# Kernel optimization log

Measured on AMD Instinct MI355X. Metric: run time of the kernel, lower is better.

Reference implementation:

```python
import jax, jax.numpy as jnp
import numpy as np

N = 207      # node_size (METR-LA)
E = 1722     # edge_size from edge CSV
RES = 12     # resolution
T = 288 // RES  # time-of-day slots


def setup_inputs() -> dict:
    key = jax.random.key(0)
    ks = jax.random.split(key, 12)
    B, L = 64, 2048
    return {
        "inputs": jax.random.normal(ks[0], (B, 2, N, L), jnp.float32),
        "ind": jax.random.randint(ks[1], (B,), 0, 288),
        "edge_from": jax.random.randint(ks[2], (E,), 0, N),
        "edge_to": jax.random.randint(ks[3], (E,), 0, N),
        "weight_react": jax.random.normal(ks[4], (T, E), jnp.float32) / 10.0,
        "weight_diff": jax.random.normal(ks[5], (T, E), jnp.float32) / 1000.0,
        "weight_react_a": jax.random.normal(ks[6], (T, E), jnp.float32) / 10.0,
        "weight_diff_a": jax.random.normal(ks[7], (T, E), jnp.float32) / 1000.0,
        "bias_reaction": jax.random.normal(ks[8], (T, N), jnp.float32) / 10.0,
        "bias_diffusion": jax.random.normal(ks[9], (T, N), jnp.float32) / 10.0,
        "bias_reaction_a": jax.random.normal(ks[10], (T, N), jnp.float32) / 10.0,
        "bias_diffusion_a": jax.random.normal(ks[11], (T, N), jnp.float32) / 10.0,
    }


def _scatter(w, src, dst):
    # dense NxN from edge list; duplicate edges accumulate (torch sparse coalesce semantics)
    return jnp.zeros((N, N), w.dtype).at[src, dst].add(w)


def _diag_colsum(A):
    # torch.sum(A, 1) on [1,N,N] sums over the first node axis -> column sums
    return jax.vmap(jnp.diag)(A.sum(axis=1))


def reference(inputs, ind, edge_from, edge_to,
              weight_react, weight_diff, weight_react_a, weight_diff_a,
              bias_reaction, bias_diffusion, bias_reaction_a, bias_diffusion_a):
    x = inputs[:, 0, :, :]              # [B, N, L]
    ii = ind // RES                      # [B] time-slot indices

    scat = jax.vmap(_scatter, in_axes=(0, None, None))
    Ar = scat(weight_react[ii], edge_from, edge_to)      # [B,N,N] index = (i, j)
    Ad = scat(weight_diff[ii], edge_to, edge_from)       # index_a = (j, i)
    Ara = scat(weight_react_a[ii], edge_from, edge_to)
    Ada = scat(weight_diff_a[ii], edge_to, edge_from)

    RW = _diag_colsum(Ar) - Ar           # Laplacian: D - A
    DW = _diag_colsum(Ad) - Ad
    RWa = _diag_colsum(Ara) + Ara        # D + A
    # faithful replication: batch element 0 uses diag of colsums of the already-built
    # reaction Laplacian (I1 - A) instead of reaction_weight_a (original-code quirk)
    RWa = RWa.at[0].set(jnp.diag(RW[0].sum(axis=0)) + Ara[0])
    DWa = _diag_colsum(Ada) + Ada

    conv = lambda A: jnp.einsum('nvl,nwv->nwl', x, A)   # out[n,w,l] = sum_v A[n,w,v] x[n,v,l]
    reaction = conv(RW) + bias_reaction[ii][:, :, None]
    reaction_a = conv(RWa) + bias_reaction_a[ii][:, :, None]
    diffusion = conv(DW) + bias_diffusion[ii][:, :, None]
    diffusion_a = conv(DWa) + bias_diffusion_a[ii][:, :, None]

    return jnp.tanh(reaction) + jnp.tanh(reaction_a) + diffusion + diffusion_a + x
```

## Files before the change

kernel.cpp:

```cpp
#include <hip/hip_runtime.h>
#include <cstdint>
#include <cstddef>

#define NN 207
#define NE 1722
#define NT 24
#define LL 2048
#define LCC 128
#define KP  208
#define MTILES 13
#define KTILES 7
#define CH_U16 3584
#define T_U16 (MTILES * 3 * CH_U16)


typedef float    f32x4 __attribute__((ext_vector_type(4)));
typedef _Float16 half8 __attribute__((ext_vector_type(8)));

__device__ __forceinline__ unsigned short f2h(float f) {
    return __builtin_bit_cast(unsigned short, (_Float16)f);
}
__device__ __forceinline__ float tanhfast(float z) {
    return 1.0f - __fdividef(2.0f, __expf(2.0f * z) + 1.0f);
}

__global__ void k_build(const int* __restrict__ efrom, const int* __restrict__ eto,
                        const float* __restrict__ wr, const float* __restrict__ wd,
                        const float* __restrict__ wra, const float* __restrict__ wda,
                        const float* __restrict__ br, const float* __restrict__ bd,
                        const float* __restrict__ bra, const float* __restrict__ bda,
                        unsigned short* __restrict__ Wpack,
                        float4* __restrict__ cb4, float4* __restrict__ bb4) {
    const int t   = blockIdx.x / MTILES;
    const int mt  = blockIdx.x % MTILES;
    const int tid = threadIdx.x;
    __shared__ float rowbuf[3][16][KP];
    __shared__ float cs[4][16];

    float* rb = &rowbuf[0][0][0];
    for (int i = tid; i < 3 * 16 * KP; i += 256) rb[i] = 0.0f;
    if (tid < 64) ((float*)cs)[tid] = 0.0f;
    __syncthreads();

    const int mt16 = mt * 16;
    const float* wrt  = wr  + (size_t)t * NE;
    const float* wdt  = wd  + (size_t)t * NE;
    const float* wrat = wra + (size_t)t * NE;
    const float* wdat = wda + (size_t)t * NE;
    for (int e = tid; e < NE; e += 256) {
        int ef = efrom[e], et = eto[e];
        unsigned rf = (unsigned)(ef - mt16), rt = (unsigned)(et - mt16);
        bool in_f = rf < 16u, in_t = rt < 16u;
        if (in_f || in_t) {
            float w1 = wrt[e], w2 = wdt[e], w3 = wrat[e], w4 = wdat[e];
            if (in_t) {
                atomicAdd(&rowbuf[2][rt][ef], w4 - w2);
                atomicAdd(&cs[0][rt], w1);
                atomicAdd(&cs[1][rt], w3);
            }
            if (in_f) {
                atomicAdd(&rowbuf[0][rf][et], -w1);
                atomicAdd(&rowbuf[1][rf][et],  w3);
                atomicAdd(&cs[2][rf], w2);
                atomicAdd(&cs[3][rf], w4);
            }
        }
    }
    __syncthreads();

    if (tid < 16) {
        int w = mt16 + tid;
        if (w < NN) {
            cb4[t * NN + w] = make_float4(cs[0][tid], cs[1][tid], cs[2][tid] + cs[3][tid], 0.0f);
            bb4[t * NN + w] = make_float4(br[t * NN + w], bra[t * NN + w],
                                          bd[t * NN + w] + bda[t * NN + w], 0.0f);
        }
    }

    for (int fr = tid; fr < 3 * KTILES * 64; fr += 256) {
        int mat = fr / (KTILES * 64);
        int rem = fr - mat * (KTILES * 64);
        int ks = rem >> 6, lq = rem & 63;
        int r = lq & 15, g = lq >> 4;
        const float* src = &rowbuf[mat][r][0];
        int k0 = ks * 32 + 4 * g;
        unsigned short h[8];
        #pragma unroll
        for (int e2 = 0; e2 < 4; ++e2) {
            h[e2] = f2h(src[k0 + e2]);
            int kb = k0 + 16 + e2;
            h[4 + e2] = (kb < KP) ? f2h(src[kb]) : (unsigned short)0;
        }
        uint4 pv;
        pv.x = (unsigned)h[0] | ((unsigned)h[1] << 16);
        pv.y = (unsigned)h[2] | ((unsigned)h[3] << 16);
        pv.z = (unsigned)h[4] | ((unsigned)h[5] << 16);
        pv.w = (unsigned)h[6] | ((unsigned)h[7] << 16);
        size_t o = ((size_t)(t * MTILES + mt) * 3 + mat) * CH_U16 + (size_t)ks * 512 + (size_t)lq * 8;
        *(uint4*)(Wpack + o) = pv;
    }
}

__global__ __launch_bounds__(512, 4) void k_mfma(
    const float* __restrict__ inputs, const int* __restrict__ ind,
    const unsigned short* __restrict__ Wpack,
    const float4* __restrict__ cb4, const float4* __restrict__ bb4,
    float* __restrict__ out) {
    __shared__ unsigned short xs[KP * LCC];
    const int b = blockIdx.y, chunk = blockIdx.x, tid = threadIdx.x;
    const int t = ind[b] / 12;

    if (tid < 64) ((unsigned*)(xs + 207 * LCC))[tid] = 0u;

    const float* xb = inputs + (size_t)b * (2 * NN * LL) + (size_t)chunk * LCC;
    for (int i = tid; i < 207 * 32; i += 512) {
        int k  = i >> 5;
        int c4 = (i & 31) << 2;
        float4 v = *(const float4*)(xb + (size_t)k * LL + c4);
        int gk = (k >> 2) & 3;
        ushort4 h;
        h.x = f2h(v.x); h.y = f2h(v.y); h.z = f2h(v.z); h.w = f2h(v.w);
        *(ushort4*)&xs[k * LCC + (c4 ^ (gk << 4))] = h;
    }
    __syncthreads();

    const int l  = tid & 63, wv = tid >> 6;
    const int r  = l & 15,  g  = l >> 4;
    const int col  = wv * 16 + r;
    const int colx = col ^ (g << 4);
    const _Float16* xh = (const _Float16*)xs;

    half8 bf[KTILES];
    #pragma unroll
    for (int ks = 0; ks < KTILES - 1; ++ks) {
        half8 v;
        int k0 = ks * 32 + 4 * g;
        #pragma unroll
        for (int e = 0; e < 4; ++e) {
            v[e]     = xh[(k0 + e) * LCC + colx];
            v[4 + e] = xh[(k0 + 16 + e) * LCC + colx];
        }
        bf[ks] = v;
    }
    {
        half8 v = {0, 0, 0, 0, 0, 0, 0, 0};
        int k0 = 192 + 4 * g;
        #pragma unroll
        for (int e = 0; e < 4; ++e) v[e] = xh[(k0 + e) * LCC + colx];
        bf[KTILES - 1] = v;
    }

    const unsigned short* Ap = Wpack + (size_t)t * T_U16 + (size_t)l * 8;
    const float4* cbp = cb4 + (size_t)t * NN;
    const float4* bbp = bb4 + (size_t)t * NN;
    float* ob = out + (size_t)b * ((size_t)NN * LL) + (size_t)chunk * LCC + col;

    for (int mt = 0; mt < MTILES; ++mt) {
        f32x4 aR = {0.f, 0.f, 0.f, 0.f};
        f32x4 aA = {0.f, 0.f, 0.f, 0.f};
        f32x4 aD = {0.f, 0.f, 0.f, 0.f};
        #pragma unroll
        for (int ks = 0; ks < KTILES; ++ks) {
            half8 a = __builtin_bit_cast(half8, *(const uint4*)(Ap + ks * 512));
            aR = __builtin_amdgcn_mfma_f32_16x16x32_f16(a, bf[ks], aR, 0, 0, 0);
        }
        #pragma unroll
        for (int ks = 0; ks < KTILES; ++ks) {
            half8 a = __builtin_bit_cast(half8, *(const uint4*)(Ap + CH_U16 + ks * 512));
            aA = __builtin_amdgcn_mfma_f32_16x16x32_f16(a, bf[ks], aA, 0, 0, 0);
        }
        #pragma unroll
        for (int ks = 0; ks < KTILES; ++ks) {
            half8 a = __builtin_bit_cast(half8, *(const uint4*)(Ap + 2 * CH_U16 + ks * 512));
            aD = __builtin_amdgcn_mfma_f32_16x16x32_f16(a, bf[ks], aD, 0, 0, 0);
        }
        Ap += 3 * CH_U16;

        const int rowb = mt * 16 + 4 * g;
        #pragma unroll
        for (int q = 0; q < 4; ++q) {
            int row = rowb + q;
            if (row < NN) {
                float xq = (float)xh[row * LCC + colx];
                float4 cb = cbp[row], bb = bbp[row];
                float rr = aR[q] + cb.x * xq + bb.x;
                float ra = aA[q] + bb.y;
                if (b != 0) ra += cb.y * xq;
                float dd = aD[q] + cb.z * xq + bb.z;
                ob[(size_t)row * LL] = tanhfast(rr) + tanhfast(ra) + dd + xq;
            }
        }
    }
}

extern "C" void kernel_launch(void* const* d_in, const int* in_sizes, int n_in,
                              void* d_out, int out_size, void* d_ws, size_t ws_size,
                              hipStream_t stream) {
    const float* inputs = (const float*)d_in[0];
    const int*   ind    = (const int*)d_in[1];
    const int*   efrom  = (const int*)d_in[2];
    const int*   eto    = (const int*)d_in[3];
    const float* wr     = (const float*)d_in[4];
    const float* wd     = (const float*)d_in[5];
    const float* wra    = (const float*)d_in[6];
    const float* wda    = (const float*)d_in[7];
    const float* br     = (const float*)d_in[8];
    const float* bd     = (const float*)d_in[9];
    const float* bra    = (const float*)d_in[10];
    const float* bda    = (const float*)d_in[11];
    float* out = (float*)d_out;

    char* ws = (char*)d_ws;
    float4*         cb4   = (float4*)(ws + 0);
    float4*         bb4   = (float4*)(ws + 79488);
    unsigned short* Wpack = (unsigned short*)(ws + 158976);

    const int B = in_sizes[1];

    k_build<<<dim3(NT * MTILES), dim3(256), 0, stream>>>(
        efrom, eto, wr, wd, wra, wda, br, bd, bra, bda, Wpack, cb4, bb4);
    k_mfma<<<dim3(LL / LCC, B), dim3(512), 0, stream>>>(
        inputs, ind, Wpack, cb4, bb4, out);
}
```

Measured before the change: 421.6 us.

## Stage x through small per-k-slice LDS buffer and reuse fragments for epilogue

Replaces the full 208x128 fp16 LDS tile with a 32-row staging buffer that is filled and consumed once per k-slice, cutting LDS use from about 53KB to 8KB so more blocks can be resident per CU. The epilogue now takes the residual x value from the already-loaded B fragments instead of rereading LDS, and the m-tile loop is fully unrolled so those fragment indices are compile-time constants. The cost is two barriers per k-slice and serialized global loads with less overlap, plus higher register pressure and code size from the unroll.

```diff
diff --git a/kernel.cpp b/kernel.cpp
--- a/kernel.cpp
+++ b/kernel.cpp
@@ -106,48 +106,40 @@
     const unsigned short* __restrict__ Wpack,
     const float4* __restrict__ cb4, const float4* __restrict__ bb4,
     float* __restrict__ out) {
-    __shared__ unsigned short xs[KP * LCC];
+    __shared__ unsigned short sl[32 * LCC];
     const int b = blockIdx.y, chunk = blockIdx.x, tid = threadIdx.x;
     const int t = ind[b] / 12;
-
-    if (tid < 64) ((unsigned*)(xs + 207 * LCC))[tid] = 0u;
-
-    const float* xb = inputs + (size_t)b * (2 * NN * LL) + (size_t)chunk * LCC;
-    for (int i = tid; i < 207 * 32; i += 512) {
-        int k  = i >> 5;
-        int c4 = (i & 31) << 2;
-        float4 v = *(const float4*)(xb + (size_t)k * LL + c4);
-        int gk = (k >> 2) & 3;
-        ushort4 h;
-        h.x = f2h(v.x); h.y = f2h(v.y); h.z = f2h(v.z); h.w = f2h(v.w);
-        *(ushort4*)&xs[k * LCC + (c4 ^ (gk << 4))] = h;
-    }
-    __syncthreads();
 
     const int l  = tid & 63, wv = tid >> 6;
     const int r  = l & 15,  g  = l >> 4;
     const int col  = wv * 16 + r;
     const int colx = col ^ (g << 4);
-    const _Float16* xh = (const _Float16*)xs;
+    const _Float16* sh = (const _Float16*)sl;
+    const float* xb = inputs + (size_t)b * (2 * NN * LL) + (size_t)chunk * LCC;
 
     half8 bf[KTILES];
-    #pragma unroll
-    for (int ks = 0; ks < KTILES - 1; ++ks) {
+    for (int ks = 0; ks < KTILES; ++ks) {
+        for (int i = tid; i < 32 * 32; i += 512) {
+            int kk = i >> 5;
+            int c4 = (i & 31) << 2;
+            int kglob = ks * 32 + kk;
+            ushort4 h = make_ushort4(0, 0, 0, 0);
+            if (kglob < NN) {
+                float4 v = *(const float4*)(xb + (size_t)kglob * LL + c4);
+                h.x = f2h(v.x); h.y = f2h(v.y); h.z = f2h(v.z); h.w = f2h(v.w);
+            }
+            *(ushort4*)&sl[kk * LCC + (c4 ^ ((((unsigned)kk >> 2) & 3u) << 4))] = h;
+        }
+        __syncthreads();
         half8 v;
-        int k0 = ks * 32 + 4 * g;
+        int k0 = 4 * g;
         #pragma unroll
         for (int e = 0; e < 4; ++e) {
-            v[e]     = xh[(k0 + e) * LCC + colx];
-            v[4 + e] = xh[(k0 + 16 + e) * LCC + colx];
+            v[e]     = sh[(k0 + e) * LCC + colx];
+            v[4 + e] = sh[(k0 + 16 + e) * LCC + colx];
         }
         bf[ks] = v;
-    }
-    {
-        half8 v = {0, 0, 0, 0, 0, 0, 0, 0};
-        int k0 = 192 + 4 * g;
-        #pragma unroll
-        for (int e = 0; e < 4; ++e) v[e] = xh[(k0 + e) * LCC + colx];
-        bf[KTILES - 1] = v;
+        __syncthreads();
     }
 
     const unsigned short* Ap = Wpack + (size_t)t * T_U16 + (size_t)l * 8;
@@ -155,6 +147,7 @@
     const float4* bbp = bb4 + (size_t)t * NN;
     float* ob = out + (size_t)b * ((size_t)NN * LL) + (size_t)chunk * LCC + col;
 
+    #pragma unroll
     for (int mt = 0; mt < MTILES; ++mt) {
         f32x4 aR = {0.f, 0.f, 0.f, 0.f};
         f32x4 aA = {0.f, 0.f, 0.f, 0.f};
@@ -181,7 +174,7 @@
         for (int q = 0; q < 4; ++q) {
             int row = rowb + q;
             if (row < NN) {
-                float xq = (float)xh[row * LCC + colx];
+                float xq = (float)bf[mt >> 1][(mt & 1) * 4 + q];
                 float4 cb = cbp[row], bb = bbp[row];
                 float rr = aR[q] + cb.x * xq + bb.x;
                 float ra = aA[q] + bb.y;
```

Result: slower. 590.2 us (+40.0%).
